# Performance work log

Measured on AMD Instinct MI355X. Metric: run time of the kernel, lower is better.

The kernel has to match this reference:

```python
import jax, jax.numpy as jnp
import numpy as np

B, T, I, H, HOUT = 512, 256, 32, 128, 1
H2 = H // 2


def setup_inputs() -> dict:
    key = jax.random.key(0)
    ks = jax.random.split(key, 16)
    s = lambda *shape: 1.0 / np.sqrt(H)
    def u(k, shape):
        return jax.random.uniform(k, shape, jnp.float32, -1.0 / np.sqrt(H), 1.0 / np.sqrt(H))
    return {
        "x": jax.random.normal(ks[0], (B, T, I), jnp.float32),
        # layer 0 LSTM weights (PyTorch layout: [4H, in], gate order i,f,g,o)
        "w_ih0": u(ks[1], (4 * H, I)),
        "w_hh0": u(ks[2], (4 * H, H)),
        "b_ih0": u(ks[3], (4 * H,)),
        "b_hh0": u(ks[4], (4 * H,)),
        # layer 1 LSTM weights
        "w_ih1": u(ks[5], (4 * H, H)),
        "w_hh1": u(ks[6], (4 * H, H)),
        "b_ih1": u(ks[7], (4 * H,)),
        "b_hh1": u(ks[8], (4 * H,)),
        # MLP head: Linear(H, H//2) -> ReLU -> Linear(H//2, HOUT)
        "fc1_w": u(ks[9], (H2, H)),
        "fc1_b": u(ks[10], (H2,)),
        "fc2_w": u(ks[11], (HOUT, H2)),
        "fc2_b": u(ks[12], (HOUT,)),
    }


def _lstm_layer(x, w_ih, w_hh, b_ih, b_hh):
    # x: (B, T, in) -> h sequence (B, T, H). Dropout is eval-mode identity.
    b, t, _ = x.shape
    h_dim = w_hh.shape[1]
    # precompute input-to-gate projections for the whole sequence (one big GEMM)
    xg = jnp.einsum("bti,gi->btg", x, w_ih) + b_ih + b_hh  # (B, T, 4H)
    xg = jnp.swapaxes(xg, 0, 1)  # (T, B, 4H) for scan

    def step(carry, g_t):
        h, c = carry
        gates = g_t + h @ w_hh.T  # (B, 4H)
        i, f, g, o = jnp.split(gates, 4, axis=-1)  # PyTorch gate order i,f,g,o
        i = jax.nn.sigmoid(i)
        f = jax.nn.sigmoid(f)
        g = jnp.tanh(g)
        o = jax.nn.sigmoid(o)
        c_new = f * c + i * g
        h_new = o * jnp.tanh(c_new)
        return (h_new, c_new), h_new

    zeros = jnp.zeros((b, h_dim), x.dtype)
    _, hs = jax.lax.scan(step, (zeros, zeros), xg)
    return jnp.swapaxes(hs, 0, 1)  # (B, T, H)


def reference(x, w_ih0, w_hh0, b_ih0, b_hh0, w_ih1, w_hh1, b_ih1, b_hh1,
              fc1_w, fc1_b, fc2_w, fc2_b):
    h0 = _lstm_layer(x, w_ih0, w_hh0, b_ih0, b_hh0)   # (B, T, H)
    h1 = _lstm_layer(h0, w_ih1, w_hh1, b_ih1, b_hh1)  # (B, T, H)
    last = h1[:, -1, :]  # (B, H); dropout = identity in eval
    z = jax.nn.relu(last @ fc1_w.T + fc1_b)  # (B, H//2)
    return z @ fc2_w.T + fc2_b  # (B, forecast_horizon)
```

## Files before the change

kernel.cpp:

```cpp
#include <hip/hip_runtime.h>

#define NB 512
#define NT 256
#define NI 32
#define NH 128
#define NG 512

typedef __attribute__((ext_vector_type(8))) short bf16x8;
typedef __attribute__((ext_vector_type(4))) float f32x4;

__device__ __forceinline__ float fsig(float x) {
    return __builtin_amdgcn_rcpf(1.0f + __expf(-x));
}
__device__ __forceinline__ float ftanh(float x) {
    float e = __expf(-2.0f * x);
    return 2.0f * __builtin_amdgcn_rcpf(1.0f + e) - 1.0f;
}
__device__ __forceinline__ unsigned short f2bf_rne(float f) {
    unsigned u = __float_as_uint(f);
    return (unsigned short)((u + 0x7FFFu + ((u >> 16) & 1u)) >> 16);
}
__device__ __forceinline__ void split2(float a, float b, unsigned& hi, unsigned& lo) {
    unsigned short ha = f2bf_rne(a), hb = f2bf_rne(b);
    float ra = a - __uint_as_float((unsigned)ha << 16);
    float rb = b - __uint_as_float((unsigned)hb << 16);
    hi = (unsigned)ha | ((unsigned)hb << 16);
    lo = (unsigned)f2bf_rne(ra) | ((unsigned)f2bf_rne(rb) << 16);
}
__device__ __forceinline__ bf16x8 u4bf(uint4 u) {
    union { uint4 u; bf16x8 v; } c; c.u = u; return c.v;
}
#define MFMA16(accv, av, bv) \
    accv = __builtin_amdgcn_mfma_f32_16x16x32_bf16(av, bv, accv, 0, 0, 0)

__device__ __forceinline__ void lds_barrier() {
    asm volatile("s_waitcnt lgkmcnt(0)\n\ts_barrier" ::: "memory");
}

__global__ __launch_bounds__(512, 1)
void recur_pair(const float* __restrict__ xg0,
                const float* __restrict__ xg1,
                const float* __restrict__ w_hh0,
                const float* __restrict__ w_hh1,
                float* __restrict__ h0buf,
                float* __restrict__ h0s, float* __restrict__ c0s,
                float* __restrict__ h1s, float* __restrict__ c1s,
                int Tc, int doA, int doB, int firstA, int firstB)
{
    __shared__ __align__(16) unsigned short Hh[2][16][128];
    __shared__ __align__(16) unsigned short Hl[2][16][128];

    const int role = blockIdx.x >> 5;
    if (role == 0 && !doA) return;
    if (role == 1 && !doB) return;

    const float* xg    = role ? xg1   : xg0;
    const float* wsrc  = role ? w_hh1 : w_hh0;
    float*       hout  = role ? nullptr : h0buf;
    float*       hs    = role ? h1s : h0s;
    float*       cs    = role ? c1s : c0s;
    const int    first = role ? firstB : firstA;

    const int p    = blockIdx.x & 31;
    const int tid  = threadIdx.x;
    const int wv   = tid >> 6;
    const int lane = tid & 63;
    const int quad = lane >> 4;
    const int ml   = lane & 15;
    const int j    = 16 * wv + ml;

    bf16x8 wh[4][4], wl[4][4];
#pragma unroll
    for (int t = 0; t < 4; ++t) {
#pragma unroll
        for (int q = 0; q < 4; ++q) {
            int n = (t * 8 + wv) * 16 + ml;
            const float* s = wsrc + (size_t)n * NH + q * 32 + quad * 8;
            float4 v0 = *(const float4*)s;
            float4 v1 = *(const float4*)(s + 4);
            uint4 H, L;
            split2(v0.x, v0.y, H.x, L.x); split2(v0.z, v0.w, H.y, L.y);
            split2(v1.x, v1.y, H.z, L.z); split2(v1.z, v1.w, H.w, L.w);
            wh[t][q] = u4bf(H);
            wl[t][q] = u4bf(L);
        }
    }

    int ro[4];
#pragma unroll
    for (int q = 0; q < 4; ++q)
        ro[q] = ((ml * 256 + q * 64 + quad * 16) ^ ((ml & 7) << 4));
    int wo[4];
    size_t hb_r[4], sb_r[4];
#pragma unroll
    for (int r = 0; r < 4; ++r) {
        int m = quad * 4 + r;
        wo[r]   = ((m * 256 + j * 2) ^ ((m & 7) << 4));
        hb_r[r] = (size_t)(p * 16 + m) * Tc * NH + j;
        sb_r[r] = (size_t)(p * 16 + m) * NH + j;
    }

    const size_t rs = (size_t)Tc * NG;
    const size_t rowb0 = ((size_t)(p * 16 + quad * 4) * Tc) * NG + j;

    float xga[4][4], xgb[4][4];
#pragma unroll
    for (int t = 0; t < 4; ++t)
#pragma unroll
        for (int r = 0; r < 4; ++r)
            xga[t][r] = xg[rowb0 + (size_t)r * rs + t * 128];

    float cr[4];
#pragma unroll
    for (int r = 0; r < 4; ++r) {
        float h = 0.f, c = 0.f;
        if (!first) {
            h = hs[sb_r[r]];
            c = cs[sb_r[r]];
        }
        cr[r] = c;
        unsigned short hi = f2bf_rne(h);
        float res = h - __uint_as_float((unsigned)hi << 16);
        unsigned short lo = f2bf_rne(res);
        *(unsigned short*)((char*)&Hh[0][0][0] + wo[r]) = hi;
        *(unsigned short*)((char*)&Hl[0][0][0] + wo[r]) = lo;
    }
    __syncthreads();

    auto prefetch = [&](float (&dst)[4][4], int tlx) __attribute__((always_inline)) {
        int tc_ = tlx < Tc ? tlx : Tc - 1;
        const size_t rowb = rowb0 + (size_t)tc_ * NG;
#pragma unroll
        for (int t = 0; t < 4; ++t)
#pragma unroll
            for (int r = 0; r < 4; ++r)
                dst[t][r] = xg[rowb + (size_t)r * rs + t * 128];
    };

    auto step_body = [&](int TL, int BUF, const float (&xgv)[4][4]) __attribute__((always_inline)) {
        const char* hb = (const char*)&Hh[BUF][0][0];
        const char* lb = (const char*)&Hl[BUF][0][0];
        char* hbn = (char*)&Hh[BUF ^ 1][0][0];
        char* lbn = (char*)&Hl[BUF ^ 1][0][0];

        f32x4 acc[4] = {};
#pragma unroll
        for (int q = 0; q < 4; ++q) {
            bf16x8 ah = *(const bf16x8*)(hb + ro[q]);
            bf16x8 al = *(const bf16x8*)(lb + ro[q]);
#pragma unroll
            for (int t = 0; t < 4; ++t) {
                MFMA16(acc[t], ah, wh[t][q]);
                MFMA16(acc[t], al, wh[t][q]);
                MFMA16(acc[t], ah, wl[t][q]);
            }
        }

#pragma unroll
        for (int r = 0; r < 4; ++r) {
            float gi = fsig (acc[0][r] + xgv[0][r]);
            float gf = fsig (acc[1][r] + xgv[1][r]);
            float gg = ftanh(acc[2][r] + xgv[2][r]);
            float go = fsig (acc[3][r] + xgv[3][r]);
            cr[r] = gf * cr[r] + gi * gg;
            float hn = go * ftanh(cr[r]);
            unsigned short hi = f2bf_rne(hn);
            float res = hn - __uint_as_float((unsigned)hi << 16);
            unsigned short lo = f2bf_rne(res);
            *(unsigned short*)(hbn + wo[r]) = hi;
            *(unsigned short*)(lbn + wo[r]) = lo;
            if (hout)
                hout[hb_r[r] + (size_t)TL * NH] = hn;
            if (TL == Tc - 1) {
                hs[sb_r[r]] = hn;
                cs[sb_r[r]] = cr[r];
            }
        }
    };

    for (int tl = 0; tl < Tc; tl += 2) {
        prefetch(xgb, tl + 1);
        step_body(tl, 0, xga);
        lds_barrier();
        if (tl + 1 < Tc) {
            prefetch(xga, tl + 2);
            step_body(tl + 1, 1, xgb);
            lds_barrier();
        }
    }
}

template<int KP, bool SLICED>
__global__ __launch_bounds__(256)
void gemm_mfma(const float* __restrict__ A,
               const float* __restrict__ Bw,
               const float* __restrict__ bi, const float* __restrict__ bh,
               float* __restrict__ C, int t0, int tcShift)
{
    constexpr int K = KP * 32;
    __shared__ __align__(16) unsigned short Ah[4][128][8], Al[4][128][8];
    __shared__ __align__(16) unsigned short Bh[4][64][8],  Bl[4][64][8];
    const int tid  = threadIdx.x;
    const int n0   = blockIdx.x * 64;
    const int m0   = blockIdx.y * 128;
    const int wv   = tid >> 6;
    const int lane = tid & 63;
    const int quad = lane >> 4, ml = lane & 15;

    f32x4 acc[2][4] = {};
    float bias[4];
#pragma unroll
    for (int nt = 0; nt < 4; ++nt) {
        int n = n0 + nt * 16 + ml;
        bias[nt] = bi[n] + bh[n];
    }

    for (int kp = 0; kp < KP; ++kp) {
        if (kp) __syncthreads();
#pragma unroll
        for (int r = 0; r < 2; ++r) {
            int u = tid + 256 * r;
            int m = u >> 2, ck = u & 3;
            size_t abase;
            if (SLICED) {
                int mg = m0 + m;
                int b  = mg >> tcShift, tl = mg & ((1 << tcShift) - 1);
                abase = ((size_t)b * NT + (t0 + tl)) * K;
            } else {
                abase = (size_t)(m0 + m) * K;
            }
            const float* s = A + abase + kp * 32 + ck * 8;
            float4 v0 = *(const float4*)s;
            float4 v1 = *(const float4*)(s + 4);
            uint4 H, L;
            split2(v0.x, v0.y, H.x, L.x); split2(v0.z, v0.w, H.y, L.y);
            split2(v1.x, v1.y, H.z, L.z); split2(v1.z, v1.w, H.w, L.w);
            *(uint4*)&Ah[ck][m][0] = H;
            *(uint4*)&Al[ck][m][0] = L;
        }
        {
            int n = tid >> 2, ck = tid & 3;
            const float* s = Bw + (size_t)(n0 + n) * K + kp * 32 + ck * 8;
            float4 v0 = *(const float4*)s;
            float4 v1 = *(const float4*)(s + 4);
            uint4 H, L;
            split2(v0.x, v0.y, H.x, L.x); split2(v0.z, v0.w, H.y, L.y);
            split2(v1.x, v1.y, H.z, L.z); split2(v1.z, v1.w, H.w, L.w);
            *(uint4*)&Bh[ck][n][0] = H;
            *(uint4*)&Bl[ck][n][0] = L;
        }
        __syncthreads();

        bf16x8 ah0 = *(const bf16x8*)&Ah[quad][(2 * wv + 0) * 16 + ml][0];
        bf16x8 al0 = *(const bf16x8*)&Al[quad][(2 * wv + 0) * 16 + ml][0];
        bf16x8 ah1 = *(const bf16x8*)&Ah[quad][(2 * wv + 1) * 16 + ml][0];
        bf16x8 al1 = *(const bf16x8*)&Al[quad][(2 * wv + 1) * 16 + ml][0];
#pragma unroll
        for (int nt = 0; nt < 4; ++nt) {
            bf16x8 bhv = *(const bf16x8*)&Bh[quad][nt * 16 + ml][0];
            bf16x8 blv = *(const bf16x8*)&Bl[quad][nt * 16 + ml][0];
            MFMA16(acc[0][nt], ah0, bhv);
            MFMA16(acc[0][nt], ah0, blv);
            MFMA16(acc[0][nt], al0, bhv);
            MFMA16(acc[1][nt], ah1, bhv);
            MFMA16(acc[1][nt], ah1, blv);
            MFMA16(acc[1][nt], al1, bhv);
        }
    }

#pragma unroll
    for (int mt = 0; mt < 2; ++mt)
#pragma unroll
        for (int nt = 0; nt < 4; ++nt)
#pragma unroll
            for (int reg = 0; reg < 4; ++reg) {
                int m = m0 + (2 * wv + mt) * 16 + quad * 4 + reg;
                int n = n0 + nt * 16 + ml;
                C[(size_t)m * NG + n] = acc[mt][nt][reg] + bias[nt];
            }
}

__global__ void fc_head(const float* __restrict__ h1,
                        const float* __restrict__ fc1w, const float* __restrict__ fc1b,
                        const float* __restrict__ fc2w, const float* __restrict__ fc2b,
                        float* __restrict__ out)
{
    int b = blockIdx.x, j = threadIdx.x;
    const float4* wr = (const float4*)(fc1w + (size_t)j * NH);
    const float4* hv = (const float4*)(h1 + (size_t)b * NH);
    float acc = fc1b[j];
#pragma unroll
    for (int q = 0; q < 32; ++q) {
        float4 w = wr[q], h = hv[q];
        acc += w.x * h.x + w.y * h.y + w.z * h.z + w.w * h.w;
    }
    float z = fmaxf(acc, 0.0f);
    float p = fc2w[j] * z;
#pragma unroll
    for (int off = 32; off > 0; off >>= 1) p += __shfl_down(p, off);
    if (j == 0) out[b] = p + fc2b[0];
}

extern "C" void kernel_launch(void* const* d_in, const int* in_sizes, int n_in,
                              void* d_out, int out_size, void* d_ws, size_t ws_size,
                              hipStream_t stream)
{
    const float* x     = (const float*)d_in[0];
    const float* w_ih0 = (const float*)d_in[1];
    const float* w_hh0 = (const float*)d_in[2];
    const float* b_ih0 = (const float*)d_in[3];
    const float* b_hh0 = (const float*)d_in[4];
    const float* w_ih1 = (const float*)d_in[5];
    const float* w_hh1 = (const float*)d_in[6];
    const float* b_ih1 = (const float*)d_in[7];
    const float* b_hh1 = (const float*)d_in[8];
    const float* fc1w  = (const float*)d_in[9];
    const float* fc1b  = (const float*)d_in[10];
    const float* fc2w  = (const float*)d_in[11];
    const float* fc2b  = (const float*)d_in[12];
    float* out = (float*)d_out;
    float* ws  = (float*)d_ws;

    int Tc = 1;
    for (int cand = 256; cand >= 1; cand >>= 1) {
        size_t need = 4ull * ((size_t)NB * cand * (2 * NG + NH) + 4ull * NB * NH);
        if (need <= ws_size) { Tc = cand; break; }
    }
    int tcShift = __builtin_ctz((unsigned)Tc);

    size_t o_xg0 = 0;
    size_t o_xg1 = o_xg0 + (size_t)NB * Tc * NG;
    size_t o_h0  = o_xg1 + (size_t)NB * Tc * NG;
    size_t o_h0s = o_h0  + (size_t)NB * Tc * NH;
    size_t o_c0s = o_h0s + (size_t)NB * NH;
    size_t o_h1s = o_c0s + (size_t)NB * NH;
    size_t o_c1s = o_h1s + (size_t)NB * NH;

    const int M = NB * Tc;
    const int nchunk = NT / Tc;

    gemm_mfma<1, true><<<dim3(8, M / 128), 256, 0, stream>>>(
        x, w_ih0, b_ih0, b_hh0, ws + o_xg0, 0, tcShift);

    for (int i = 0; i <= nchunk; ++i) {
        int doA = (i < nchunk), doB = (i >= 1);
        recur_pair<<<64, 512, 0, stream>>>(
            ws + o_xg0, ws + o_xg1, w_hh0, w_hh1, ws + o_h0,
            ws + o_h0s, ws + o_c0s, ws + o_h1s, ws + o_c1s,
            Tc, doA, doB, i == 0, i == 1);
        if (i < nchunk)
            gemm_mfma<4, false><<<dim3(8, M / 128), 256, 0, stream>>>(
                ws + o_h0, w_ih1, b_ih1, b_hh1, ws + o_xg1, 0, 0);
        if (i + 1 < nchunk)
            gemm_mfma<1, true><<<dim3(8, M / 128), 256, 0, stream>>>(
                x, w_ih0, b_ih0, b_hh0, ws + o_xg0, (i + 1) * Tc, tcShift);
    }
    fc_head<<<NB, 64, 0, stream>>>(ws + o_h1s, fc1w, fc1b, fc2w, fc2b, out);
}
```

Measured before the change: 825.6 us.

## Fuse LSTM pipeline into one persistent cooperative kernel with grid barriers

Replaces the per-chunk launches of the recurrence, the two input-projection GEMMs and the FC head with a single cooperative kernel. Inside it, 64 blocks run the two recurrent layers while the other blocks compute the layer-1 and layer-0 projections into double-buffered chunks, with atomic grid barriers between chunks. The aim is to remove launch overhead and overlap the GEMMs with the recurrence. The gate activations now fold log2(e) scaling and the sign into the weights and projections, so each gate needs fewer exp/rcp operations. The MFMA accumulation is split across two accumulators to shorten dependency chains. In exchange it adds grid-wide spin barriers and a fixed chunk size, and the FC head is folded in at the end.

```diff
diff --git a/kernel.cpp b/kernel.cpp
--- a/kernel.cpp
+++ b/kernel.cpp
@@ -5,17 +5,21 @@
 #define NI 32
 #define NH 128
 #define NG 512
+#define TC 32
+#define NCH 8
+#define NBLK 256
+#define NWB 152
+#define NWA 40
+
+#define L2E  1.4426950408889634f
+#define L2E2 2.8853900817779268f
 
 typedef __attribute__((ext_vector_type(8))) short bf16x8;
 typedef __attribute__((ext_vector_type(4))) float f32x4;
 
-__device__ __forceinline__ float fsig(float x) {
-    return __builtin_amdgcn_rcpf(1.0f + __expf(-x));
-}
-__device__ __forceinline__ float ftanh(float x) {
-    float e = __expf(-2.0f * x);
-    return 2.0f * __builtin_amdgcn_rcpf(1.0f + e) - 1.0f;
-}
+constexpr size_t XGCH = (size_t)NB * TC * NG;
+constexpr size_t H0CH = (size_t)NB * TC * NH;
+
 __device__ __forceinline__ unsigned short f2bf_rne(float f) {
     unsigned u = __float_as_uint(f);
     return (unsigned short)((u + 0x7FFFu + ((u >> 16) & 1u)) >> 16);
@@ -37,268 +41,282 @@
     asm volatile("s_waitcnt lgkmcnt(0)\n\ts_barrier" ::: "memory");
 }
 
+__device__ __forceinline__ void gsync(unsigned* ctr) {
+    __threadfence();
+    __syncthreads();
+    if (threadIdx.x == 0) {
+        __hip_atomic_fetch_add(ctr, 1u, __ATOMIC_ACQ_REL, __HIP_MEMORY_SCOPE_AGENT);
+        while (__hip_atomic_load(ctr, __ATOMIC_ACQUIRE, __HIP_MEMORY_SCOPE_AGENT)
+               < (unsigned)NBLK)
+            __builtin_amdgcn_s_sleep(1);
+    }
+    __syncthreads();
+    __threadfence();
+}
+
 __global__ __launch_bounds__(512, 1)
-void recur_pair(const float* __restrict__ xg0,
-                const float* __restrict__ xg1,
-                const float* __restrict__ w_hh0,
-                const float* __restrict__ w_hh1,
-                float* __restrict__ h0buf,
-                float* __restrict__ h0s, float* __restrict__ c0s,
-                float* __restrict__ h1s, float* __restrict__ c1s,
-                int Tc, int doA, int doB, int firstA, int firstB)
+void mega(const float* __restrict__ x,
+          const float* __restrict__ w_hh0, const float* __restrict__ w_hh1,
+          const float* __restrict__ w_ih0, const float* __restrict__ b_ih0,
+          const float* __restrict__ b_hh0,
+          const float* __restrict__ w_ih1, const float* __restrict__ b_ih1,
+          const float* __restrict__ b_hh1,
+          const float* __restrict__ fc1w, const float* __restrict__ fc1b,
+          const float* __restrict__ fc2w, const float* __restrict__ fc2b,
+          float* __restrict__ xg0, float* __restrict__ xg1,
+          float* __restrict__ h0,  float* __restrict__ h1s,
+          float* __restrict__ out, unsigned* __restrict__ bar)
 {
     __shared__ __align__(16) unsigned short Hh[2][16][128];
     __shared__ __align__(16) unsigned short Hl[2][16][128];
-
-    const int role = blockIdx.x >> 5;
-    if (role == 0 && !doA) return;
-    if (role == 1 && !doB) return;
-
-    const float* xg    = role ? xg1   : xg0;
-    const float* wsrc  = role ? w_hh1 : w_hh0;
-    float*       hout  = role ? nullptr : h0buf;
-    float*       hs    = role ? h1s : h0s;
-    float*       cs    = role ? c1s : c0s;
-    const int    first = role ? firstB : firstA;
-
-    const int p    = blockIdx.x & 31;
+    __shared__ __align__(16) unsigned short GAh[4][128][8], GAl[4][128][8];
+    __shared__ __align__(16) unsigned short GBh[4][64][8],  GBl[4][64][8];
+
+    const int bid  = blockIdx.x;
     const int tid  = threadIdx.x;
     const int wv   = tid >> 6;
     const int lane = tid & 63;
     const int quad = lane >> 4;
     const int ml   = lane & 15;
-    const int j    = 16 * wv + ml;
-
-    bf16x8 wh[4][4], wl[4][4];
-#pragma unroll
-    for (int t = 0; t < 4; ++t) {
-#pragma unroll
-        for (int q = 0; q < 4; ++q) {
-            int n = (t * 8 + wv) * 16 + ml;
-            const float* s = wsrc + (size_t)n * NH + q * 32 + quad * 8;
-            float4 v0 = *(const float4*)s;
-            float4 v1 = *(const float4*)(s + 4);
-            uint4 H, L;
-            split2(v0.x, v0.y, H.x, L.x); split2(v0.z, v0.w, H.y, L.y);
-            split2(v1.x, v1.y, H.z, L.z); split2(v1.z, v1.w, H.w, L.w);
-            wh[t][q] = u4bf(H);
-            wl[t][q] = u4bf(L);
-        }
+
+    if (bid < 64) {
+        const int role = bid >> 5;
+        const int p    = bid & 31;
+        const int j    = 16 * wv + ml;
+        const float* wsrc = role ? w_hh1 : w_hh0;
+
+        bf16x8 wh[4][4], wl[4][4];
+#pragma unroll
+        for (int t = 0; t < 4; ++t) {
+            const float sc = (t == 2) ? L2E2 : L2E;
+#pragma unroll
+            for (int q = 0; q < 4; ++q) {
+                int n = (t * 8 + wv) * 16 + ml;
+                const float* s = wsrc + (size_t)n * NH + q * 32 + quad * 8;
+                float4 v0 = *(const float4*)s;
+                float4 v1 = *(const float4*)(s + 4);
+                uint4 H, L;
+                split2(v0.x * sc, v0.y * sc, H.x, L.x); split2(v0.z * sc, v0.w * sc, H.y, L.y);
+                split2(v1.x * sc, v1.y * sc, H.z, L.z); split2(v1.z * sc, v1.w * sc, H.w, L.w);
+                wh[t][q] = u4bf(H);
+                wl[t][q] = u4bf(L);
+            }
+        }
+
+        int ro[4];
+#pragma unroll
+        for (int q = 0; q < 4; ++q)
+            ro[q] = ((ml * 256 + q * 64 + quad * 16) ^ ((ml & 7) << 4));
+        int wo[4];
+        size_t hb_r[4], sb_r[4];
+#pragma unroll
+        for (int r = 0; r < 4; ++r) {
+            int m = quad * 4 + r;
+            wo[r]   = ((m * 256 + j * 2) ^ ((m & 7) << 4));
+            hb_r[r] = (size_t)(p * 16 + m) * TC * NH + j;
+            sb_r[r] = (size_t)(p * 16 + m) * NH + j;
+        }
+
+        float cr[4] = {};
+#pragma unroll
+        for (int r = 0; r < 4; ++r) {
+            *(unsigned short*)((char*)&Hh[0][0][0] + wo[r]) = 0;
+            *(unsigned short*)((char*)&Hl[0][0][0] + wo[r]) = 0;
+        }
+        __syncthreads();
+
+        auto activ = [&](float mi, float mf, float mg, float mo, float& c)
+            __attribute__((always_inline)) -> float {
+            float ei = exp2f(mi), ef = exp2f(mf), eg = exp2f(mg), eo = exp2f(mo);
+            float rf  = __builtin_amdgcn_rcpf(1.0f + ef);
+            float rig = __builtin_amdgcn_rcpf((1.0f + ei) * (1.0f + eg));
+            float cn  = c * rf + (1.0f - eg) * rig;
+            c = cn;
+            float ec = exp2f(cn * -L2E2);
+            float rh = __builtin_amdgcn_rcpf((1.0f + eo) * (1.0f + ec));
+            return (1.0f - ec) * rh;
+        };
+
+        const size_t rs    = (size_t)TC * NG;
+        const size_t rowb0 = ((size_t)(p * 16 + quad * 4) * TC) * NG + j;
+
+        for (int i = -1; i <= NCH + 1; ++i) {
+            const int c = role ? i - 2 : i;
+            if (c >= 0 && c < NCH) {
+                const float* xg   = (role ? xg1 : xg0) + (size_t)(c & 1) * XGCH;
+                float*       hout = role ? nullptr : h0 + (size_t)(c & 1) * H0CH;
+                const bool   last = role && (c == NCH - 1);
+
+                auto prefetch = [&](float (&dst)[4][4], int tlx)
+                    __attribute__((always_inline)) {
+                    int tc_ = tlx < TC ? tlx : TC - 1;
+                    const size_t rowb = rowb0 + (size_t)tc_ * NG;
+#pragma unroll
+                    for (int t = 0; t < 4; ++t)
+#pragma unroll
+                        for (int r = 0; r < 4; ++r)
+                            dst[t][r] = xg[rowb + (size_t)r * rs + t * 128];
+                };
+
+                auto step = [&](int TL, int BUF, const float (&xgv)[4][4])
+                    __attribute__((always_inline)) {
+                    const char* hb = (const char*)&Hh[BUF][0][0];
+                    const char* lb = (const char*)&Hl[BUF][0][0];
+                    char* hbn = (char*)&Hh[BUF ^ 1][0][0];
+                    char* lbn = (char*)&Hl[BUF ^ 1][0][0];
+
+                    f32x4 P[4] = {}, Q[4] = {};
+#pragma unroll
+                    for (int q = 0; q < 4; ++q) {
+                        bf16x8 ah = *(const bf16x8*)(hb + ro[q]);
+                        bf16x8 al = *(const bf16x8*)(lb + ro[q]);
+#pragma unroll
+                        for (int t = 0; t < 4; ++t) {
+                            MFMA16(P[t], ah, wh[t][q]);
+                            MFMA16(Q[t], al, wh[t][q]);
+                            if (q & 1) { MFMA16(P[t], ah, wl[t][q]); }
+                            else       { MFMA16(Q[t], ah, wl[t][q]); }
+                        }
+                    }
+#pragma unroll
+                    for (int r = 0; r < 4; ++r) {
+                        float mi = xgv[0][r] - P[0][r] - Q[0][r];
+                        float mf = xgv[1][r] - P[1][r] - Q[1][r];
+                        float mg = xgv[2][r] - P[2][r] - Q[2][r];
+                        float mo = xgv[3][r] - P[3][r] - Q[3][r];
+                        float hn = activ(mi, mf, mg, mo, cr[r]);
+                        unsigned short hi = f2bf_rne(hn);
+                        float res = hn - __uint_as_float((unsigned)hi << 16);
+                        unsigned short lo = f2bf_rne(res);
+                        *(unsigned short*)(hbn + wo[r]) = hi;
+                        *(unsigned short*)(lbn + wo[r]) = lo;
+                        if (hout)
+                            hout[hb_r[r] + (size_t)TL * NH] = hn;
+                        if (last && TL == TC - 1)
+                            h1s[sb_r[r]] = hn;
+                    }
+                };
+
+                float xga[4][4], xgb[4][4];
+                prefetch(xga, 0);
+                for (int tl = 0; tl < TC; tl += 2) {
+                    prefetch(xgb, tl + 1);
+                    step(tl, 0, xga);
+                    lds_barrier();
+                    prefetch(xga, tl + 2);
+                    step(tl + 1, 1, xgb);
+                    lds_barrier();
+                }
+            }
+            gsync(&bar[i + 1]);
+        }
+
+        if (role == 0) {
+            const int g = tid >> 5;
+            const int l = tid & 31;
+            const float4* h4 = (const float4*)(h1s + (size_t)(p * 16 + g) * NH);
+            const float4* w0 = (const float4*)(fc1w + (size_t)l * NH);
+            const float4* w1 = (const float4*)(fc1w + (size_t)(l + 32) * NH);
+            float a0 = fc1b[l], a1 = fc1b[l + 32];
+#pragma unroll
+            for (int q = 0; q < 32; ++q) {
+                float4 h = h4[q], u = w0[q], v = w1[q];
+                a0 += u.x * h.x + u.y * h.y + u.z * h.z + u.w * h.w;
+                a1 += v.x * h.x + v.y * h.y + v.z * h.z + v.w * h.w;
+            }
+            float pv = fc2w[l] * fmaxf(a0, 0.f) + fc2w[l + 32] * fmaxf(a1, 0.f);
+#pragma unroll
+            for (int off = 16; off > 0; off >>= 1) pv += __shfl_down(pv, off, 32);
+            if (l == 0) out[p * 16 + g] = pv + fc2b[0];
+        }
+        return;
     }
 
-    int ro[4];
-#pragma unroll
-    for (int q = 0; q < 4; ++q)
-        ro[q] = ((ml * 256 + q * 64 + quad * 16) ^ ((ml & 7) << 4));
-    int wo[4];
-    size_t hb_r[4], sb_r[4];
-#pragma unroll
-    for (int r = 0; r < 4; ++r) {
-        int m = quad * 4 + r;
-        wo[r]   = ((m * 256 + j * 2) ^ ((m & 7) << 4));
-        hb_r[r] = (size_t)(p * 16 + m) * Tc * NH + j;
-        sb_r[r] = (size_t)(p * 16 + m) * NH + j;
+    const int w = bid - 64;
+
+    auto gemm_run = [&](const float* __restrict__ A, const float* __restrict__ Bw,
+                        const float* __restrict__ bi, const float* __restrict__ bh,
+                        float* __restrict__ C, int t0, int wk, int nw,
+                        int KP, bool SLICED) __attribute__((always_inline)) {
+        const int AS = SLICED ? NI : NH;
+        for (int tile = wk; tile < 1024; tile += nw) {
+            const int n0 = (tile & 7) * 64;
+            const int m0 = (tile >> 3) * 128;
+            const float s = ((n0 >> 7) == 2) ? L2E2 : L2E;
+            f32x4 acc[4] = {};
+            for (int kp = 0; kp < KP; ++kp) {
+                __syncthreads();
+                {
+                    int m = tid >> 2, ck = tid & 3;
+                    size_t abase;
+                    if (SLICED) {
+                        int mg = m0 + m;
+                        int b  = mg >> 5, tl = mg & 31;
+                        abase = ((size_t)b * NT + (t0 + tl)) * AS;
+                    } else {
+                        abase = (size_t)(m0 + m) * AS;
+                    }
+                    const float* sp = A + abase + kp * 32 + ck * 8;
+                    float4 v0 = *(const float4*)sp;
+                    float4 v1 = *(const float4*)(sp + 4);
+                    uint4 H, L;
+                    split2(v0.x, v0.y, H.x, L.x); split2(v0.z, v0.w, H.y, L.y);
+                    split2(v1.x, v1.y, H.z, L.z); split2(v1.z, v1.w, H.w, L.w);
+                    *(uint4*)&GAh[ck][m][0] = H;
+                    *(uint4*)&GAl[ck][m][0] = L;
+                }
+                if (tid < 256) {
+                    int n = tid >> 2, ck = tid & 3;
+                    const float* sp = Bw + (size_t)(n0 + n) * AS + kp * 32 + ck * 8;
+                    float4 v0 = *(const float4*)sp;
+                    float4 v1 = *(const float4*)(sp + 4);
+                    uint4 H, L;
+                    split2(v0.x, v0.y, H.x, L.x); split2(v0.z, v0.w, H.y, L.y);
+                    split2(v1.x, v1.y, H.z, L.z); split2(v1.z, v1.w, H.w, L.w);
+                    *(uint4*)&GBh[ck][n][0] = H;
+                    *(uint4*)&GBl[ck][n][0] = L;
+                }
+                __syncthreads();
+
+                bf16x8 ah = *(const bf16x8*)&GAh[quad][wv * 16 + ml][0];
+                bf16x8 al = *(const bf16x8*)&GAl[quad][wv * 16 + ml][0];
+#pragma unroll
+                for (int nt = 0; nt < 4; ++nt) {
+                    bf16x8 bhv = *(const bf16x8*)&GBh[quad][nt * 16 + ml][0];
+                    bf16x8 blv = *(const bf16x8*)&GBl[quad][nt * 16 + ml][0];
+                    MFMA16(acc[nt], ah, bhv);
+                    MFMA16(acc[nt], ah, blv);
+                    MFMA16(acc[nt], al, bhv);
+                }
+            }
+#pragma unroll
+            for (int nt = 0; nt < 4; ++nt) {
+                int n = n0 + nt * 16 + ml;
+                float nb = -(bi[n] + bh[n]) * s;
+#pragma unroll
+                for (int reg = 0; reg < 4; ++reg) {
+                    int m = m0 + wv * 16 + quad * 4 + reg;
+                    C[(size_t)m * NG + n] = fmaf(acc[nt][reg], -s, nb);
+                }
+            }
+        }
+    };
+
+    for (int i = -1; i <= NCH + 1; ++i) {
+        if (w < NWB) {
+            const int c1 = i - 1;
+            if (c1 >= 0 && c1 < NCH)
+                gemm_run(h0 + (size_t)(c1 & 1) * H0CH, w_ih1, b_ih1, b_hh1,
+                         xg1 + (size_t)(c1 & 1) * XGCH, 0, w, NWB, 4, false);
+        } else {
+            const int c2 = i + 1;
+            if (c2 < NCH)
+                gemm_run(x, w_ih0, b_ih0, b_hh0,
+                         xg0 + (size_t)(c2 & 1) * XGCH, c2 * TC, w - NWB, NWA,
+                         1, true);
+        }
+        gsync(&bar[i + 1]);
     }
-
-    const size_t rs = (size_t)Tc * NG;
-    const size_t rowb0 = ((size_t)(p * 16 + quad * 4) * Tc) * NG + j;
-
-    float xga[4][4], xgb[4][4];
-#pragma unroll
-    for (int t = 0; t < 4; ++t)
-#pragma unroll
-        for (int r = 0; r < 4; ++r)
-            xga[t][r] = xg[rowb0 + (size_t)r * rs + t * 128];
-
-    float cr[4];
-#pragma unroll
-    for (int r = 0; r < 4; ++r) {
-        float h = 0.f, c = 0.f;
-        if (!first) {
-            h = hs[sb_r[r]];
-            c = cs[sb_r[r]];
-        }
-        cr[r] = c;
-        unsigned short hi = f2bf_rne(h);
-        float res = h - __uint_as_float((unsigned)hi << 16);
-        unsigned short lo = f2bf_rne(res);
-        *(unsigned short*)((char*)&Hh[0][0][0] + wo[r]) = hi;
-        *(unsigned short*)((char*)&Hl[0][0][0] + wo[r]) = lo;
-    }
-    __syncthreads();
-
-    auto prefetch = [&](float (&dst)[4][4], int tlx) __attribute__((always_inline)) {
-        int tc_ = tlx < Tc ? tlx : Tc - 1;
-        const size_t rowb = rowb0 + (size_t)tc_ * NG;
-#pragma unroll
-        for (int t = 0; t < 4; ++t)
-#pragma unroll
-            for (int r = 0; r < 4; ++r)
-                dst[t][r] = xg[rowb + (size_t)r * rs + t * 128];
-    };
-
-    auto step_body = [&](int TL, int BUF, const float (&xgv)[4][4]) __attribute__((always_inline)) {
-        const char* hb = (const char*)&Hh[BUF][0][0];
-        const char* lb = (const char*)&Hl[BUF][0][0];
-        char* hbn = (char*)&Hh[BUF ^ 1][0][0];
-        char* lbn = (char*)&Hl[BUF ^ 1][0][0];
-
-        f32x4 acc[4] = {};
-#pragma unroll
-        for (int q = 0; q < 4; ++q) {
-            bf16x8 ah = *(const bf16x8*)(hb + ro[q]);
-            bf16x8 al = *(const bf16x8*)(lb + ro[q]);
-#pragma unroll
-            for (int t = 0; t < 4; ++t) {
-                MFMA16(acc[t], ah, wh[t][q]);
-                MFMA16(acc[t], al, wh[t][q]);
-                MFMA16(acc[t], ah, wl[t][q]);
-            }
-        }
-
-#pragma unroll
-        for (int r = 0; r < 4; ++r) {
-            float gi = fsig (acc[0][r] + xgv[0][r]);
-            float gf = fsig (acc[1][r] + xgv[1][r]);
-            float gg = ftanh(acc[2][r] + xgv[2][r]);
-            float go = fsig (acc[3][r] + xgv[3][r]);
-            cr[r] = gf * cr[r] + gi * gg;
-            float hn = go * ftanh(cr[r]);
-            unsigned short hi = f2bf_rne(hn);
-            float res = hn - __uint_as_float((unsigned)hi << 16);
-            unsigned short lo = f2bf_rne(res);
-            *(unsigned short*)(hbn + wo[r]) = hi;
-            *(unsigned short*)(lbn + wo[r]) = lo;
-            if (hout)
-                hout[hb_r[r] + (size_t)TL * NH] = hn;
-            if (TL == Tc - 1) {
-                hs[sb_r[r]] = hn;
-                cs[sb_r[r]] = cr[r];
-            }
-        }
-    };
-
-    for (int tl = 0; tl < Tc; tl += 2) {
-        prefetch(xgb, tl + 1);
-        step_body(tl, 0, xga);
-        lds_barrier();
-        if (tl + 1 < Tc) {
-            prefetch(xga, tl + 2);
-            step_body(tl + 1, 1, xgb);
-            lds_barrier();
-        }
-    }
-}
-
-template<int KP, bool SLICED>
-__global__ __launch_bounds__(256)
-void gemm_mfma(const float* __restrict__ A,
-               const float* __restrict__ Bw,
-               const float* __restrict__ bi, const float* __restrict__ bh,
-               float* __restrict__ C, int t0, int tcShift)
-{
-    constexpr int K = KP * 32;
-    __shared__ __align__(16) unsigned short Ah[4][128][8], Al[4][128][8];
-    __shared__ __align__(16) unsigned short Bh[4][64][8],  Bl[4][64][8];
-    const int tid  = threadIdx.x;
-    const int n0   = blockIdx.x * 64;
-    const int m0   = blockIdx.y * 128;
-    const int wv   = tid >> 6;
-    const int lane = tid & 63;
-    const int quad = lane >> 4, ml = lane & 15;
-
-    f32x4 acc[2][4] = {};
-    float bias[4];
-#pragma unroll
-    for (int nt = 0; nt < 4; ++nt) {
-        int n = n0 + nt * 16 + ml;
-        bias[nt] = bi[n] + bh[n];
-    }
-
-    for (int kp = 0; kp < KP; ++kp) {
-        if (kp) __syncthreads();
-#pragma unroll
-        for (int r = 0; r < 2; ++r) {
-            int u = tid + 256 * r;
-            int m = u >> 2, ck = u & 3;
-            size_t abase;
-            if (SLICED) {
-                int mg = m0 + m;
-                int b  = mg >> tcShift, tl = mg & ((1 << tcShift) - 1);
-                abase = ((size_t)b * NT + (t0 + tl)) * K;
-            } else {
-                abase = (size_t)(m0 + m) * K;
-            }
-            const float* s = A + abase + kp * 32 + ck * 8;
-            float4 v0 = *(const float4*)s;
-            float4 v1 = *(const float4*)(s + 4);
-            uint4 H, L;
-            split2(v0.x, v0.y, H.x, L.x); split2(v0.z, v0.w, H.y, L.y);
-            split2(v1.x, v1.y, H.z, L.z); split2(v1.z, v1.w, H.w, L.w);
-            *(uint4*)&Ah[ck][m][0] = H;
-            *(uint4*)&Al[ck][m][0] = L;
-        }
-        {
-            int n = tid >> 2, ck = tid & 3;
-            const float* s = Bw + (size_t)(n0 + n) * K + kp * 32 + ck * 8;
-            float4 v0 = *(const float4*)s;
-            float4 v1 = *(const float4*)(s + 4);
-            uint4 H, L;
-            split2(v0.x, v0.y, H.x, L.x); split2(v0.z, v0.w, H.y, L.y);
-            split2(v1.x, v1.y, H.z, L.z); split2(v1.z, v1.w, H.w, L.w);
-            *(uint4*)&Bh[ck][n][0] = H;
-            *(uint4*)&Bl[ck][n][0] = L;
-        }
-        __syncthreads();
-
-        bf16x8 ah0 = *(const bf16x8*)&Ah[quad][(2 * wv + 0) * 16 + ml][0];
-        bf16x8 al0 = *(const bf16x8*)&Al[quad][(2 * wv + 0) * 16 + ml][0];
-        bf16x8 ah1 = *(const bf16x8*)&Ah[quad][(2 * wv + 1) * 16 + ml][0];
-        bf16x8 al1 = *(const bf16x8*)&Al[quad][(2 * wv + 1) * 16 + ml][0];
-#pragma unroll
-        for (int nt = 0; nt < 4; ++nt) {
-            bf16x8 bhv = *(const bf16x8*)&Bh[quad][nt * 16 + ml][0];
-            bf16x8 blv = *(const bf16x8*)&Bl[quad][nt * 16 + ml][0];
-            MFMA16(acc[0][nt], ah0, bhv);
-            MFMA16(acc[0][nt], ah0, blv);
-            MFMA16(acc[0][nt], al0, bhv);
-            MFMA16(acc[1][nt], ah1, bhv);
-            MFMA16(acc[1][nt], ah1, blv);
-            MFMA16(acc[1][nt], al1, bhv);
-        }
-    }
-
-#pragma unroll
-    for (int mt = 0; mt < 2; ++mt)
-#pragma unroll
-        for (int nt = 0; nt < 4; ++nt)
-#pragma unroll
-            for (int reg = 0; reg < 4; ++reg) {
-                int m = m0 + (2 * wv + mt) * 16 + quad * 4 + reg;
-                int n = n0 + nt * 16 + ml;
-                C[(size_t)m * NG + n] = acc[mt][nt][reg] + bias[nt];
-            }
-}
-
-__global__ void fc_head(const float* __restrict__ h1,
-                        const float* __restrict__ fc1w, const float* __restrict__ fc1b,
-                        const float* __restrict__ fc2w, const float* __restrict__ fc2b,
-                        float* __restrict__ out)
-{
-    int b = blockIdx.x, j = threadIdx.x;
-    const float4* wr = (const float4*)(fc1w + (size_t)j * NH);
-    const float4* hv = (const float4*)(h1 + (size_t)b * NH);
-    float acc = fc1b[j];
-#pragma unroll
-    for (int q = 0; q < 32; ++q) {
-        float4 w = wr[q], h = hv[q];
-        acc += w.x * h.x + w.y * h.y + w.z * h.z + w.w * h.w;
-    }
-    float z = fmaxf(acc, 0.0f);
-    float p = fc2w[j] * z;
-#pragma unroll
-    for (int off = 32; off > 0; off >>= 1) p += __shfl_down(p, off);
-    if (j == 0) out[b] = p + fc2b[0];
 }
 
 extern "C" void kernel_launch(void* const* d_in, const int* in_sizes, int n_in,
@@ -321,39 +339,29 @@
     float* out = (float*)d_out;
     float* ws  = (float*)d_ws;
 
-    int Tc = 1;
-    for (int cand = 256; cand >= 1; cand >>= 1) {
-        size_t need = 4ull * ((size_t)NB * cand * (2 * NG + NH) + 4ull * NB * NH);
-        if (need <= ws_size) { Tc = cand; break; }
-    }
-    int tcShift = __builtin_ctz((unsigned)Tc);
-
     size_t o_xg0 = 0;
-    size_t o_xg1 = o_xg0 + (size_t)NB * Tc * NG;
-    size_t o_h0  = o_xg1 + (size_t)NB * Tc * NG;
-    size_t o_h0s = o_h0  + (size_t)NB * Tc * NH;
-    size_t o_c0s = o_h0s + (size_t)NB * NH;
-    size_t o_h1s = o_c0s + (size_t)NB * NH;
-    size_t o_c1s = o_h1s + (size_t)NB * NH;
-
-    const int M = NB * Tc;
-    const int nchunk = NT / Tc;
-
-    gemm_mfma<1, true><<<dim3(8, M / 128), 256, 0, stream>>>(
-        x, w_ih0, b_ih0, b_hh0, ws + o_xg0, 0, tcShift);
-
-    for (int i = 0; i <= nchunk; ++i) {
-        int doA = (i < nchunk), doB = (i >= 1);
-        recur_pair<<<64, 512, 0, stream>>>(
-            ws + o_xg0, ws + o_xg1, w_hh0, w_hh1, ws + o_h0,
-            ws + o_h0s, ws + o_c0s, ws + o_h1s, ws + o_c1s,
-            Tc, doA, doB, i == 0, i == 1);
-        if (i < nchunk)
-            gemm_mfma<4, false><<<dim3(8, M / 128), 256, 0, stream>>>(
-                ws + o_h0, w_ih1, b_ih1, b_hh1, ws + o_xg1, 0, 0);
-        if (i + 1 < nchunk)
-            gemm_mfma<1, true><<<dim3(8, M / 128), 256, 0, stream>>>(
-                x, w_ih0, b_ih0, b_hh0, ws + o_xg0, (i + 1) * Tc, tcShift);
-    }
-    fc_head<<<NB, 64, 0, stream>>>(ws + o_h1s, fc1w, fc1b, fc2w, fc2b, out);
-}
+    size_t o_xg1 = o_xg0 + 2 * XGCH;
+    size_t o_h0  = o_xg1 + 2 * XGCH;
+    size_t o_h1s = o_h0  + 2 * H0CH;
+    size_t o_bar = o_h1s + (size_t)NB * NH;
+
+    float* xg0p = ws + o_xg0;
+    float* xg1p = ws + o_xg1;
+    float* h0p  = ws + o_h0;
+    float* h1sp = ws + o_h1s;
+    unsigned* barp = (unsigned*)(ws + o_bar);
+
+    hipMemsetAsync(barp, 0, 64 * sizeof(unsigned), stream);
+
+    void* args[] = {
+        (void*)&x,
+        (void*)&w_hh0, (void*)&w_hh1,
+        (void*)&w_ih0, (void*)&b_ih0, (void*)&b_hh0,
+        (void*)&w_ih1, (void*)&b_ih1, (void*)&b_hh1,
+        (void*)&fc1w, (void*)&fc1b, (void*)&fc2w, (void*)&fc2b,
+        (void*)&xg0p, (void*)&xg1p, (void*)&h0p, (void*)&h1sp,
+        (void*)&out, (void*)&barp,
+    };
+    hipLaunchCooperativeKernel((const void*)mega, dim3(NBLK), dim3(512),
+                               args, 0, stream);
+}
```

Measured after the change: 2.518 ms. 3.05x slower.
